# Kernel optimization log

Hardware: AMD Instinct MI355X
Metric: run time of the kernel (lower is better)

Reference implementation:

```python
import jax, jax.numpy as jnp
import numpy as np

V, D, H, L, DFF = 32000, 512, 8, 6, 2048
B, T = 64, 256
PAD_IDX = 1


def _pos_encoding(t, d):
    pos = jnp.arange(t, dtype=jnp.float32)[:, None]          # [t,1]
    i2 = jnp.arange(0, d, 2, dtype=jnp.float32)              # [d/2]
    ang = pos / jnp.power(10000.0, i2 / d)                   # [t,d/2]
    pe = jnp.zeros((t, d), dtype=jnp.float32)
    pe = pe.at[:, 0::2].set(jnp.sin(ang))
    pe = pe.at[:, 1::2].set(jnp.cos(ang))
    return pe


def _ln(x, g, b):
    mu = x.mean(-1, keepdims=True)
    var = ((x - mu) ** 2).mean(-1, keepdims=True)
    return (x - mu) * jax.lax.rsqrt(var + 1e-5) * g + b


def _mha(xq, xkv, Wq, Wk, Wv, Wo, bo, causal):
    b, tq, d = xq.shape
    tk = xkv.shape[1]
    hd = d // H
    q = (xq @ Wq).reshape(b, tq, H, hd)
    k = (xkv @ Wk).reshape(b, tk, H, hd)
    v = (xkv @ Wv).reshape(b, tk, H, hd)
    wei = jnp.einsum('bqhd,bkhd->bhqk', q, k) * (hd ** -0.5)
    if causal:
        mask = jnp.tril(jnp.ones((tq, tk), dtype=bool))
        wei = jnp.where(mask, wei, -jnp.inf)
    wei = jax.nn.softmax(wei, axis=-1)
    out = jnp.einsum('bhqk,bkhd->bqhd', wei, v).reshape(b, tq, d)
    return out @ Wo + bo


def _ffn(x, W1, b1, W2, b2):
    return jax.nn.relu(x @ W1 + b1) @ W2 + b2


def setup_inputs() -> dict:
    key = jax.random.key(0)
    ks = iter(jax.random.split(key, 64))
    nrm = lambda shape: (jax.random.normal(next(ks), shape, dtype=jnp.float32) * 0.02)
    inp = {
        'idx': jax.random.randint(next(ks), (B, T), 0, V),
        'idx_enc': jax.random.randint(next(ks), (B, T), 0, V),
        'targets': jax.random.randint(next(ks), (B, T), 0, V),
        'emb_dec': nrm((V, D)),
        'emb_enc': nrm((V, D)),
        # encoder stacks [L, ...]
        'enc_Wq': nrm((L, D, D)), 'enc_Wk': nrm((L, D, D)), 'enc_Wv': nrm((L, D, D)),
        'enc_Wo': nrm((L, D, D)), 'enc_bo': jnp.zeros((L, D)),
        'enc_ln_g': jnp.ones((L, 2, D)), 'enc_ln_b': jnp.zeros((L, 2, D)),
        'enc_W1': nrm((L, D, DFF)), 'enc_b1': jnp.zeros((L, DFF)),
        'enc_W2': nrm((L, DFF, D)), 'enc_b2': jnp.zeros((L, D)),
        # decoder stacks [L, ...]
        'dec_Wq_sa': nrm((L, D, D)), 'dec_Wk_sa': nrm((L, D, D)), 'dec_Wv_sa': nrm((L, D, D)),
        'dec_Wo_sa': nrm((L, D, D)), 'dec_bo_sa': jnp.zeros((L, D)),
        'dec_Wq_xa': nrm((L, D, D)), 'dec_Wk_xa': nrm((L, D, D)), 'dec_Wv_xa': nrm((L, D, D)),
        'dec_Wo_xa': nrm((L, D, D)), 'dec_bo_xa': jnp.zeros((L, D)),
        'dec_ln_g': jnp.ones((L, 4, D)), 'dec_ln_b': jnp.zeros((L, 4, D)),
        'dec_W1': nrm((L, D, DFF)), 'dec_b1': jnp.zeros((L, DFF)),
        'dec_W2': nrm((L, DFF, D)), 'dec_b2': jnp.zeros((L, D)),
        'lnf_g': jnp.ones((D,)), 'lnf_b': jnp.zeros((D,)),
        'Wlm': nrm((D, V)), 'blm': jnp.zeros((V,)),
    }
    return inp


def reference(idx, idx_enc, targets, emb_dec, emb_enc,
              enc_Wq, enc_Wk, enc_Wv, enc_Wo, enc_bo, enc_ln_g, enc_ln_b,
              enc_W1, enc_b1, enc_W2, enc_b2,
              dec_Wq_sa, dec_Wk_sa, dec_Wv_sa, dec_Wo_sa, dec_bo_sa,
              dec_Wq_xa, dec_Wk_xa, dec_Wv_xa, dec_Wo_xa, dec_bo_xa,
              dec_ln_g, dec_ln_b, dec_W1, dec_b1, dec_W2, dec_b2,
              lnf_g, lnf_b, Wlm, blm):
    t_dec = idx.shape[1]
    t_enc = idx_enc.shape[1]
    pe = _pos_encoding(256, D)
    # encoder
    y = emb_enc[idx_enc] + pe[:t_enc]
    for l in range(L):
        h = _ln(y, enc_ln_g[l, 0], enc_ln_b[l, 0])
        y = y + _mha(h, h, enc_Wq[l], enc_Wk[l], enc_Wv[l], enc_Wo[l], enc_bo[l], causal=False)
        h = _ln(y, enc_ln_g[l, 1], enc_ln_b[l, 1])
        y = y + _ffn(h, enc_W1[l], enc_b1[l], enc_W2[l], enc_b2[l])
    # decoder
    x = emb_dec[idx] + pe[:t_dec]
    for l in range(L):
        h = _ln(x, dec_ln_g[l, 0], dec_ln_b[l, 0])
        x = x + _mha(h, h, dec_Wq_sa[l], dec_Wk_sa[l], dec_Wv_sa[l], dec_Wo_sa[l], dec_bo_sa[l], causal=True)
        hq = _ln(x, dec_ln_g[l, 1], dec_ln_b[l, 1])
        hk = _ln(y, dec_ln_g[l, 2], dec_ln_b[l, 2])
        x = x + _mha(hq, hk, dec_Wq_xa[l], dec_Wk_xa[l], dec_Wv_xa[l], dec_Wo_xa[l], dec_bo_xa[l], causal=False)
        h = _ln(x, dec_ln_g[l, 3], dec_ln_b[l, 3])
        x = x + _ffn(h, dec_W1[l], dec_b1[l], dec_W2[l], dec_b2[l])
    x = _ln(x, lnf_g, lnf_b)
    logits = (x @ Wlm + blm).reshape(-1, V)  # [B*T, V]
    # cross entropy with ignore_index = PAD_IDX, mean over non-ignored
    tgt = targets.reshape(-1)
    logp = jax.nn.log_softmax(logits, axis=-1)
    nll = -jnp.take_along_axis(logp, tgt[:, None], axis=-1)[:, 0]
    valid = (tgt != PAD_IDX).astype(logits.dtype)
    loss = jnp.sum(nll * valid) / jnp.maximum(jnp.sum(valid), 1.0)
    return logits, loss
```

## Files before the change

kernel.cpp:

```cpp
#include <hip/hip_runtime.h>

typedef __attribute__((ext_vector_type(8))) short s8v;
typedef __attribute__((ext_vector_type(4))) float f4v;
using u16 = unsigned short;

__device__ __forceinline__ u16 f2bf(float f) {
  union { float f; unsigned u; } v; v.f = f;
  return (u16)((v.u + 0x7FFFu + ((v.u >> 16) & 1u)) >> 16);
}

__global__ __launch_bounds__(256) void pe_kernel(float* __restrict__ pe) {
  int i = blockIdx.x * 256 + threadIdx.x;
  int t = i >> 8, p = i & 255;
  float ex = (2.f * (float)p) / 512.f;
  float ang = (float)t * expf(-ex * 9.210340371976184f);
  pe[t * 512 + 2 * p]     = sinf(ang);
  pe[t * 512 + 2 * p + 1] = cosf(ang);
}

__global__ __launch_bounds__(256) void wconv_kernel(const float* __restrict__ in,
    u16* __restrict__ out, int R, int C, size_t dstride) {
  __shared__ float tile[64][65];
  const size_t mat = (size_t)R * C;
  const float* src = in + (size_t)blockIdx.z * mat;
  u16* dst = out + (size_t)blockIdx.z * dstride;
  int r0 = blockIdx.x * 64, c0 = blockIdx.y * 64;
  int tr = threadIdx.x >> 6, tc = threadIdx.x & 63;
#pragma unroll
  for (int i = 0; i < 16; ++i)
    tile[i * 4 + tr][tc] = src[(size_t)(r0 + i * 4 + tr) * C + (c0 + tc)];
  __syncthreads();
#pragma unroll
  for (int i = 0; i < 16; ++i)
    dst[(size_t)(c0 + i * 4 + tr) * R + (r0 + tc)] = f2bf(tile[tc][i * 4 + tr]);
}

struct WcSq { const float* src[12]; u16* dst[12]; unsigned long long dstr[12]; };
__global__ __launch_bounds__(256) void wconv_sq_kernel(WcSq S) {
  __shared__ float tile[64][65];
  int mm = blockIdx.z / 6, l = blockIdx.z % 6;
  const float* src = S.src[mm] + (size_t)l * 512 * 512;
  u16* dst = S.dst[mm] + (size_t)l * S.dstr[mm];
  int r0 = blockIdx.x * 64, c0 = blockIdx.y * 64;
  int tr = threadIdx.x >> 6, tc = threadIdx.x & 63;
#pragma unroll
  for (int i = 0; i < 16; ++i)
    tile[i * 4 + tr][tc] = src[(size_t)(r0 + i * 4 + tr) * 512 + (c0 + tc)];
  __syncthreads();
#pragma unroll
  for (int i = 0; i < 16; ++i)
    dst[(size_t)(c0 + i * 4 + tr) * 512 + (r0 + tc)] = f2bf(tile[tc][i * 4 + tr]);
}

__device__ __forceinline__ void ln_row(f4v v0, f4v v1, const float* g, const float* b,
                                       int lane, u16* outrow) {
  float s = v0[0] + v0[1] + v0[2] + v0[3] + v1[0] + v1[1] + v1[2] + v1[3];
#pragma unroll
  for (int o = 1; o < 64; o <<= 1) s += __shfl_xor(s, o);
  float mu = s * (1.f / 512.f);
  float q = 0.f;
#pragma unroll
  for (int j = 0; j < 4; ++j) {
    float d0 = v0[j] - mu; q += d0 * d0;
    float d1 = v1[j] - mu; q += d1 * d1;
  }
#pragma unroll
  for (int o = 1; o < 64; o <<= 1) q += __shfl_xor(q, o);
  float rs = rsqrtf(q * (1.f / 512.f) + 1e-5f);
  f4v g0 = *(const f4v*)(g + lane * 8), g1 = *(const f4v*)(g + lane * 8 + 4);
  f4v b0 = *(const f4v*)(b + lane * 8), b1 = *(const f4v*)(b + lane * 8 + 4);
  s8v ov;
#pragma unroll
  for (int j = 0; j < 4; ++j) {
    ov[j]     = (short)f2bf((v0[j] - mu) * rs * g0[j] + b0[j]);
    ov[4 + j] = (short)f2bf((v1[j] - mu) * rs * g1[j] + b1[j]);
  }
  *(s8v*)(outrow + lane * 8) = ov;
}

__global__ __launch_bounds__(256) void ln_kernel(const float* __restrict__ x,
    const float* __restrict__ g, const float* __restrict__ b, u16* __restrict__ out) {
  int row = blockIdx.x * 4 + (threadIdx.x >> 6);
  int lane = threadIdx.x & 63;
  const float* xr = x + (size_t)row * 512 + lane * 8;
  ln_row(*(const f4v*)xr, *(const f4v*)(xr + 4), g, b, lane, out + (size_t)row * 512);
}

__global__ __launch_bounds__(256) void ln2_kernel(
    const float* __restrict__ x1, const float* __restrict__ g1, const float* __restrict__ b1,
    u16* __restrict__ o1, const float* __restrict__ x2, const float* __restrict__ g2,
    const float* __restrict__ b2, u16* __restrict__ o2) {
  int row = blockIdx.x * 4 + (threadIdx.x >> 6);
  int lane = threadIdx.x & 63;
  const float* x = x1; const float* g = g1; const float* b = b1; u16* o = o1;
  if (row >= 16384) { row -= 16384; x = x2; g = g2; b = b2; o = o2; }
  const float* xr = x + (size_t)row * 512 + lane * 8;
  ln_row(*(const f4v*)xr, *(const f4v*)(xr + 4), g, b, lane, o + (size_t)row * 512);
}

__global__ __launch_bounds__(256) void emb_ln_kernel(const int* __restrict__ idx,
    const float* __restrict__ emb, const float* __restrict__ pe,
    const float* __restrict__ g, const float* __restrict__ b,
    float* __restrict__ y, u16* __restrict__ h) {
  int row = blockIdx.x * 4 + (threadIdx.x >> 6);
  int lane = threadIdx.x & 63;
  int tok = idx[row], t = row & 255;
  const float* e = emb + (size_t)tok * 512 + lane * 8;
  const float* p = pe + (size_t)t * 512 + lane * 8;
  f4v v0 = *(const f4v*)e + *(const f4v*)p;
  f4v v1 = *(const f4v*)(e + 4) + *(const f4v*)(p + 4);
  float* yr = y + (size_t)row * 512 + lane * 8;
  *(f4v*)yr = v0; *(f4v*)(yr + 4) = v1;
  ln_row(v0, v1, g, b, lane, h + (size_t)row * 512);
}

template<int HAS_BIAS, int ADD_RES, int RELU, int OUT_BF16, int WLOSS, int NT,
         int SWZM, int DUAL>
__global__ __launch_bounds__(256, 4) void gemm128(
    const u16* __restrict__ A, const u16* __restrict__ Bt,
    const float* __restrict__ bias, const float* __restrict__ res,
    void* __restrict__ outp, int M, int N, int K,
    float* __restrict__ pmax, float* __restrict__ psum,
    const u16* __restrict__ A2, const u16* __restrict__ Bt2,
    void* __restrict__ out2) {
  __shared__ __align__(16) u16 smem[2 * 128 * 64];
  u16* As = smem;
  u16* Bs = smem + 128 * 64;
  const int tid = threadIdx.x, lane = tid & 63, w = tid >> 6;
  int bx, by;
  if (SWZM == 1) {
    int flat = blockIdx.y * gridDim.x + blockIdx.x;
    int xcd = flat & 7, local = flat >> 3;
    int p = local / gridDim.y;
    by = local - p * gridDim.y;
    bx = xcd * (gridDim.x >> 3) + p;
  } else {
    int nx = gridDim.x;
    int flat = blockIdx.y * nx + blockIdx.x;
    int per = (nx * gridDim.y) >> 3;
    int sw = (flat & 7) * per + (flat >> 3);
    by = sw / nx; bx = sw - by * nx;
  }
  if (DUAL && by >= 4) { A = A2; Bt = Bt2; outp = out2; N = 1024; by -= 4; }
  const int m0 = bx * 128, n0 = by * 128;
  const int wm = (w >> 1) * 64, wn = (w & 1) * 64;
  const int lhi = lane >> 4, llo = lane & 15;
  const int srow = tid >> 3;
  const int sl = tid & 7;
  const int gcol = (sl ^ (srow & 7)) * 8;

  const u16* Ag = A + (size_t)(m0 + srow) * K + gcol;
  const u16* Bg = Bt + (size_t)(n0 + srow) * K + gcol;
  const size_t rstep = (size_t)32 * K;
  const int sx = llo & 7;

  f4v acc[4][4] = {};
  const int nk = K >> 6;
  for (int t = 0; t < nk; ++t) {
    const int kt = t * 64;
#pragma unroll
    for (int q = 0; q < 4; ++q)
      __builtin_amdgcn_global_load_lds(
          (const __attribute__((address_space(1))) void*)(Ag + q * rstep + kt),
          (__attribute__((address_space(3))) void*)(&As[(q * 32 + srow) * 64 + sl * 8]),
          16, 0, 0);
#pragma unroll
    for (int q = 0; q < 4; ++q)
      __builtin_amdgcn_global_load_lds(
          (const __attribute__((address_space(1))) void*)(Bg + q * rstep + kt),
          (__attribute__((address_space(3))) void*)(&Bs[(q * 32 + srow) * 64 + sl * 8]),
          16, 0, 0);
    __syncthreads();
#pragma unroll
    for (int kk = 0; kk < 2; ++kk) {
      s8v af[4], bfv[4];
#pragma unroll
      for (int i = 0; i < 4; ++i)
        af[i] = *(const s8v*)&As[(wm + i * 16 + llo) * 64 + (((kk * 4 + lhi) ^ sx) * 8)];
#pragma unroll
      for (int j = 0; j < 4; ++j)
        bfv[j] = *(const s8v*)&Bs[(wn + j * 16 + llo) * 64 + (((kk * 4 + lhi) ^ sx) * 8)];
#pragma unroll
      for (int i = 0; i < 4; ++i)
#pragma unroll
        for (int j = 0; j < 4; ++j)
          acc[i][j] = __builtin_amdgcn_mfma_f32_16x16x32_bf16(af[i], bfv[j], acc[i][j], 0, 0, 0);
    }
    __syncthreads();
  }

  if (OUT_BF16) {
    float bvj[4];
#pragma unroll
    for (int j = 0; j < 4; ++j)
      bvj[j] = HAS_BIAS ? bias[n0 + wn + j * 16 + llo] : 0.f;
#pragma unroll
    for (int i = 0; i < 4; ++i) {
#pragma unroll
      for (int j = 0; j < 4; ++j) {
        int col = n0 + wn + j * 16 + llo;
#pragma unroll
        for (int r = 0; r < 4; ++r) {
          int row = m0 + wm + i * 16 + lhi * 4 + r;
          float v = acc[i][j][r] + bvj[j];
          if (RELU) v = fmaxf(v, 0.f);
          ((u16*)outp)[(size_t)row * N + col] = f2bf(v);
        }
      }
    }
  } else {
    float* lb = (float*)smem;
    float* wbuf = lb + w * 1088;
    float* lbm = lb + 4608;
    float* lbs = lb + 4864;
    f4v bias4 = {0.f, 0.f, 0.f, 0.f};
    if (HAS_BIAS) bias4 = *(const f4v*)(bias + n0 + wn + llo * 4);
#pragma unroll
    for (int i = 0; i < 4; ++i) {
#pragma unroll
      for (int j = 0; j < 4; ++j)
#pragma unroll
        for (int r = 0; r < 4; ++r)
          wbuf[(lhi * 4 + r) * 68 + j * 16 + llo] = acc[i][j][r];
      asm volatile("s_waitcnt lgkmcnt(0)" ::: "memory");
      __builtin_amdgcn_sched_barrier(0);
#pragma unroll
      for (int p = 0; p < 4; ++p) {
        int r16 = p * 4 + lhi;
        f4v v4 = *(const f4v*)&wbuf[r16 * 68 + llo * 4];
        v4 += bias4;
        int grow = m0 + wm + i * 16 + r16;
        int gcol4 = n0 + wn + llo * 4;
        if (ADD_RES) v4 += *(const f4v*)(res + (size_t)grow * N + gcol4);
        if (RELU) {
          v4[0] = fmaxf(v4[0], 0.f); v4[1] = fmaxf(v4[1], 0.f);
          v4[2] = fmaxf(v4[2], 0.f); v4[3] = fmaxf(v4[3], 0.f);
        }
        float* dst = (float*)outp + (size_t)grow * N + gcol4;
        if (NT) __builtin_nontemporal_store(v4, (f4v*)dst);
        else    *(f4v*)dst = v4;
        if (WLOSS) {
          float mx = fmaxf(fmaxf(v4[0], v4[1]), fmaxf(v4[2], v4[3]));
          mx = fmaxf(mx, __shfl_xor(mx, 1));
          mx = fmaxf(mx, __shfl_xor(mx, 2));
          mx = fmaxf(mx, __shfl_xor(mx, 4));
          mx = fmaxf(mx, __shfl_xor(mx, 8));
          float sum = __expf(v4[0] - mx) + __expf(v4[1] - mx)
                    + __expf(v4[2] - mx) + __expf(v4[3] - mx);
          sum += __shfl_xor(sum, 1); sum += __shfl_xor(sum, 2);
          sum += __shfl_xor(sum, 4); sum += __shfl_xor(sum, 8);
          if (llo == 0) {
            int lr = wm + i * 16 + r16;
            lbm[lr * 2 + (wn >> 6)] = mx;
            lbs[lr * 2 + (wn >> 6)] = sum;
          }
        }
      }
      asm volatile("s_waitcnt lgkmcnt(0)" ::: "memory");
      __builtin_amdgcn_sched_barrier(0);
    }
    if (WLOSS) {
      __syncthreads();
      if (tid < 128) {
        float ma = lbm[tid * 2], mb = lbm[tid * 2 + 1];
        float sa = lbs[tid * 2], sb = lbs[tid * 2 + 1];
        float m = fmaxf(ma, mb);
        float ss = sa * __expf(ma - m) + sb * __expf(mb - m);
        int ntile = N >> 7;
        pmax[(size_t)(m0 + tid) * ntile + by] = m;
        psum[(size_t)(m0 + tid) * ntile + by] = ss;
      }
    }
  }
}

__global__ __launch_bounds__(256, 2) void attn_kernel(
    const u16* __restrict__ Qp, int qs, const u16* __restrict__ Kp,
    const u16* __restrict__ Vp, int kvs, u16* __restrict__ Ob, int causal) {
  __shared__ __align__(16) u16 Ks[64][72];
  __shared__ __align__(16) u16 Vt[64][66];
  __shared__ __align__(16) u16 Ps[4][16][66];
  const int tid = threadIdx.x, lane = tid & 63, w = tid >> 6;
  const int b = blockIdx.x >> 3, h = blockIdx.x & 7;
  const size_t qbase  = (size_t)b * 256 * qs  + (size_t)h * 64;
  const size_t kvbase = (size_t)b * 256 * kvs + (size_t)h * 64;
  const size_t obase  = (size_t)b * 256 * 512 + (size_t)h * 64;
  const int lhi = lane >> 4, llo = lane & 15;
  s8v aq0[4], aq1[4];
#pragma unroll
  for (int qc = 0; qc < 4; ++qc) {
    const u16* qp = Qp + qbase + (size_t)(w * 64 + qc * 16 + llo) * qs;
    aq0[qc] = *(const s8v*)(qp + lhi * 8);
    aq1[qc] = *(const s8v*)(qp + 32 + lhi * 8);
  }
  f4v o[4][4] = {};
  float mrow[16], lrow[16];
#pragma unroll
  for (int i = 0; i < 16; ++i) { mrow[i] = -1e30f; lrow[i] = 0.f; }

  for (int kt = 0; kt < 4; ++kt) {
    if (kt) __syncthreads();
    {
      int tr = tid >> 3, d0 = (tid & 7) * 8;
#pragma unroll
      for (int it = 0; it < 2; ++it) {
        int t = it * 32 + tr;
        const u16* kp = Kp + kvbase + (size_t)(kt * 64 + t) * kvs + d0;
        *(s8v*)&Ks[t][d0] = *(const s8v*)kp;
        s8v vv = *(const s8v*)(Vp + kvbase + (size_t)(kt * 64 + t) * kvs + d0);
#pragma unroll
        for (int j = 0; j < 8; ++j) Vt[d0 + j][t] = (u16)vv[j];
      }
    }
    __syncthreads();
#pragma unroll
    for (int qc = 0; qc < 4; ++qc) {
      if (causal && kt * 64 > w * 64 + qc * 16 + 15) continue;
      f4v S[4];
#pragma unroll
      for (int c = 0; c < 4; ++c) {
        s8v bk0 = *(const s8v*)&Ks[c * 16 + llo][lhi * 8];
        s8v bk1 = *(const s8v*)&Ks[c * 16 + llo][32 + lhi * 8];
        f4v z = {0.f, 0.f, 0.f, 0.f};
        z = __builtin_amdgcn_mfma_f32_16x16x32_bf16(aq0[qc], bk0, z, 0, 0, 0);
        S[c] = __builtin_amdgcn_mfma_f32_16x16x32_bf16(aq1[qc], bk1, z, 0, 0, 0);
      }
      float scv[4];
#pragma unroll
      for (int r = 0; r < 4; ++r) {
        const int tq = w * 64 + qc * 16 + lhi * 4 + r;
        float tmax = -1e30f;
#pragma unroll
        for (int c = 0; c < 4; ++c) {
          float s = S[c][r] * 0.125f;
          if (causal && (kt * 64 + c * 16 + llo) > tq) s = -1e30f;
          S[c][r] = s;
          tmax = fmaxf(tmax, s);
        }
        tmax = fmaxf(tmax, __shfl_xor(tmax, 1));
        tmax = fmaxf(tmax, __shfl_xor(tmax, 2));
        tmax = fmaxf(tmax, __shfl_xor(tmax, 4));
        tmax = fmaxf(tmax, __shfl_xor(tmax, 8));
        float mo = mrow[qc * 4 + r];
        float mn = fmaxf(mo, tmax);
        float sc = __expf(mo - mn);
        float sum = 0.f;
#pragma unroll
        for (int c = 0; c < 4; ++c) {
          float p = __expf(S[c][r] - mn);
          sum += p;
          Ps[w][lhi * 4 + r][c * 16 + llo] = f2bf(p);
        }
        sum += __shfl_xor(sum, 1); sum += __shfl_xor(sum, 2);
        sum += __shfl_xor(sum, 4); sum += __shfl_xor(sum, 8);
        lrow[qc * 4 + r] = lrow[qc * 4 + r] * sc + sum;
        mrow[qc * 4 + r] = mn;
        scv[r] = sc;
      }
#pragma unroll
      for (int nb = 0; nb < 4; ++nb)
#pragma unroll
        for (int r = 0; r < 4; ++r)
          o[qc][nb][r] *= scv[r];
      asm volatile("s_waitcnt lgkmcnt(0)" ::: "memory");
      __builtin_amdgcn_sched_barrier(0);
#pragma unroll
      for (int kb = 0; kb < 2; ++kb) {
        s8v pa = *(const s8v*)&Ps[w][llo][kb * 32 + lhi * 8];
#pragma unroll
        for (int nb = 0; nb < 4; ++nb) {
          s8v bv = *(const s8v*)&Vt[nb * 16 + llo][kb * 32 + lhi * 8];
          o[qc][nb] = __builtin_amdgcn_mfma_f32_16x16x32_bf16(pa, bv, o[qc][nb], 0, 0, 0);
        }
      }
    }
  }
#pragma unroll
  for (int qc = 0; qc < 4; ++qc)
#pragma unroll
    for (int nb = 0; nb < 4; ++nb)
#pragma unroll
      for (int r = 0; r < 4; ++r) {
        float inv = 1.f / lrow[qc * 4 + r];
        Ob[obase + (size_t)(w * 64 + qc * 16 + lhi * 4 + r) * 512 + nb * 16 + llo] =
            f2bf(o[qc][nb][r] * inv);
      }
}

__global__ __launch_bounds__(256) void loss_lse_kernel(const float* __restrict__ pmax,
    const float* __restrict__ psum, const float* __restrict__ logits,
    const int* __restrict__ tgt, float* __restrict__ nll, float* __restrict__ valid) {
  const int w = threadIdx.x >> 6, lane = threadIdx.x & 63;
  const int row = blockIdx.x * 4 + w;
  float m = -1e30f, s = 0.f;
  for (int e = lane; e < 250; e += 64) {
    float pm = pmax[(size_t)row * 250 + e], ps = psum[(size_t)row * 250 + e];
    if (pm > m) { s = s * __expf(m - pm) + ps; m = pm; }
    else          s += ps * __expf(pm - m);
  }
#pragma unroll
  for (int o = 1; o < 64; o <<= 1) {
    float om = __shfl_xor(m, o), os = __shfl_xor(s, o);
    float mm = fmaxf(m, om);
    s = s * __expf(m - mm) + os * __expf(om - mm);
    m = mm;
  }
  if (lane == 0) {
    int t = tgt[row];
    float lse = m + logf(s);
    float v = (t != 1) ? 1.f : 0.f;
    nll[row] = v * (lse - logits[(size_t)row * 32000 + t]);
    valid[row] = v;
  }
}

__global__ __launch_bounds__(256) void loss_final_kernel(const float* __restrict__ nll,
    const float* __restrict__ valid, float* __restrict__ out) {
  __shared__ float sa[256], sb[256];
  int tid = threadIdx.x;
  float s = 0.f, c = 0.f;
  for (int i = tid; i < 16384; i += 256) { s += nll[i]; c += valid[i]; }
  sa[tid] = s; sb[tid] = c;
  __syncthreads();
  for (int st = 128; st > 0; st >>= 1) {
    if (tid < st) { sa[tid] += sa[tid + st]; sb[tid] += sb[tid + st]; }
    __syncthreads();
  }
  if (tid == 0) out[0] = sa[0] / fmaxf(sb[0], 1.f);
}

extern "C" void kernel_launch(void* const* d_in, const int* in_sizes, int n_in,
                              void* d_out, int out_size, void* d_ws, size_t ws_size,
                              hipStream_t stream) {
  (void)in_sizes; (void)n_in; (void)out_size; (void)ws_size;
  const int* idx       = (const int*)d_in[0];
  const int* idx_enc   = (const int*)d_in[1];
  const int* targets   = (const int*)d_in[2];
  const float* emb_dec = (const float*)d_in[3];
  const float* emb_enc = (const float*)d_in[4];
  const float* enc_Wq  = (const float*)d_in[5];
  const float* enc_Wk  = (const float*)d_in[6];
  const float* enc_Wv  = (const float*)d_in[7];
  const float* enc_Wo  = (const float*)d_in[8];
  const float* enc_bo  = (const float*)d_in[9];
  const float* enc_ln_g = (const float*)d_in[10];
  const float* enc_ln_b = (const float*)d_in[11];
  const float* enc_W1  = (const float*)d_in[12];
  const float* enc_b1  = (const float*)d_in[13];
  const float* enc_W2  = (const float*)d_in[14];
  const float* enc_b2  = (const float*)d_in[15];
  const float* dWq_sa  = (const float*)d_in[16];
  const float* dWk_sa  = (const float*)d_in[17];
  const float* dWv_sa  = (const float*)d_in[18];
  const float* dWo_sa  = (const float*)d_in[19];
  const float* dbo_sa  = (const float*)d_in[20];
  const float* dWq_xa  = (const float*)d_in[21];
  const float* dWk_xa  = (const float*)d_in[22];
  const float* dWv_xa  = (const float*)d_in[23];
  const float* dWo_xa  = (const float*)d_in[24];
  const float* dbo_xa  = (const float*)d_in[25];
  const float* dec_ln_g = (const float*)d_in[26];
  const float* dec_ln_b = (const float*)d_in[27];
  const float* dec_W1  = (const float*)d_in[28];
  const float* dec_b1  = (const float*)d_in[29];
  const float* dec_W2  = (const float*)d_in[30];
  const float* dec_b2  = (const float*)d_in[31];
  const float* lnf_g   = (const float*)d_in[32];
  const float* lnf_b   = (const float*)d_in[33];
  const float* Wlm     = (const float*)d_in[34];
  const float* blm     = (const float*)d_in[35];
  float* out_logits = (float*)d_out;
  float* out_loss   = out_logits + (size_t)16384 * 32000;

  size_t off = 0;
  auto alloc = [&](size_t bytes) -> char* {
    char* p = (char*)d_ws + off;
    off += (bytes + 255) & ~(size_t)255;
    return p;
  };
  const size_t SQ = 512 * 512, SF = 512 * 2048;
  u16* tWqkvE = (u16*)alloc(6 * 3 * SQ * 2);
  u16* tWoE   = (u16*)alloc(6 * SQ * 2);
  u16* tW1E   = (u16*)alloc(6 * SF * 2);
  u16* tW2E   = (u16*)alloc(6 * SF * 2);
  u16* tWqkvS = (u16*)alloc(6 * 3 * SQ * 2);
  u16* tWoS   = (u16*)alloc(6 * SQ * 2);
  u16* tWqX   = (u16*)alloc(6 * SQ * 2);
  u16* tWkvX  = (u16*)alloc(6 * 2 * SQ * 2);
  u16* tWoX   = (u16*)alloc(6 * SQ * 2);
  u16* tW1D   = (u16*)alloc(6 * SF * 2);
  u16* tW2D   = (u16*)alloc(6 * SF * 2);
  u16* tWlm   = (u16*)alloc((size_t)32000 * 512 * 2);
  float* pe   = (float*)alloc(256 * 512 * 4);
  float* yE   = (float*)alloc((size_t)16384 * 512 * 4);
  float* xD   = (float*)alloc((size_t)16384 * 512 * 4);
  u16* hA     = (u16*)alloc((size_t)16384 * 512 * 2);
  u16* hB     = (u16*)alloc((size_t)16384 * 512 * 2);
  u16* qkvB   = (u16*)alloc((size_t)16384 * 1536 * 2);
  u16* qB     = (u16*)alloc((size_t)16384 * 512 * 2);
  u16* kvB    = (u16*)alloc((size_t)16384 * 1024 * 2);
  u16* atB    = (u16*)alloc((size_t)16384 * 512 * 2);
  u16* midB   = (u16*)alloc((size_t)16384 * 2048 * 2);
  float* pmax = (float*)alloc((size_t)16384 * 250 * 4);
  float* psum = (float*)alloc((size_t)16384 * 250 * 4);
  float* rnll = (float*)alloc(16384 * 4);
  float* rval = (float*)alloc(16384 * 4);

  dim3 tb(256);
  const size_t S3 = 3 * SQ, S2 = 2 * SQ;
  {
    WcSq S;
    S.src[0] = enc_Wq;  S.dst[0] = tWqkvE + 0 * SQ; S.dstr[0] = S3;
    S.src[1] = enc_Wk;  S.dst[1] = tWqkvE + 1 * SQ; S.dstr[1] = S3;
    S.src[2] = enc_Wv;  S.dst[2] = tWqkvE + 2 * SQ; S.dstr[2] = S3;
    S.src[3] = enc_Wo;  S.dst[3] = tWoE;            S.dstr[3] = SQ;
    S.src[4] = dWq_sa;  S.dst[4] = tWqkvS + 0 * SQ; S.dstr[4] = S3;
    S.src[5] = dWk_sa;  S.dst[5] = tWqkvS + 1 * SQ; S.dstr[5] = S3;
    S.src[6] = dWv_sa;  S.dst[6] = tWqkvS + 2 * SQ; S.dstr[6] = S3;
    S.src[7] = dWo_sa;  S.dst[7] = tWoS;            S.dstr[7] = SQ;
    S.src[8] = dWq_xa;  S.dst[8] = tWqX;            S.dstr[8] = SQ;
    S.src[9] = dWk_xa;  S.dst[9] = tWkvX + 0 * SQ;  S.dstr[9] = S2;
    S.src[10] = dWv_xa; S.dst[10] = tWkvX + 1 * SQ; S.dstr[10] = S2;
    S.src[11] = dWo_xa; S.dst[11] = tWoX;           S.dstr[11] = SQ;
    wconv_sq_kernel<<<dim3(8, 8, 72), tb, 0, stream>>>(S);
  }
  wconv_kernel<<<dim3(8, 32, 6), tb, 0, stream>>>(enc_W1, tW1E, 512, 2048, SF);
  wconv_kernel<<<dim3(32, 8, 6), tb, 0, stream>>>(enc_W2, tW2E, 2048, 512, SF);
  wconv_kernel<<<dim3(8, 32, 6), tb, 0, stream>>>(dec_W1, tW1D, 512, 2048, SF);
  wconv_kernel<<<dim3(32, 8, 6), tb, 0, stream>>>(dec_W2, tW2D, 2048, 512, SF);
  wconv_kernel<<<dim3(8, 500, 1), tb, 0, stream>>>(Wlm, tWlm, 512, 32000, (size_t)0);
  pe_kernel<<<256, 256, 0, stream>>>(pe);

  auto ln = [&](const float* xin, const float* g, const float* bb, u16* o) {
    ln_kernel<<<4096, 256, 0, stream>>>(xin, g, bb, o);
  };
  auto g_bf16 = [&](const u16* Ap, const u16* Bp, u16* Op, int N) {
    gemm128<0, 0, 0, 1, 0, 0, 0, 0><<<dim3(128, N / 128), 256, 0, stream>>>(
        Ap, Bp, nullptr, nullptr, Op, 16384, N, 512, nullptr, nullptr,
        nullptr, nullptr, nullptr);
  };
  auto g_qkv_x = [&](const u16* Aq, const u16* Bq, u16* Oq,
                     const u16* Akv, const u16* Bkv, u16* Okv) {
    gemm128<0, 0, 0, 1, 0, 0, 0, 1><<<dim3(128, 12), 256, 0, stream>>>(
        Aq, Bq, nullptr, nullptr, Oq, 16384, 512, 512, nullptr, nullptr,
        Akv, Bkv, Okv);
  };
  auto proj_res = [&](const u16* Ap, const u16* Bp, const float* bi, float* xr, int K) {
    gemm128<1, 1, 0, 0, 0, 0, 0, 0><<<dim3(128, 4), 256, 0, stream>>>(
        Ap, Bp, bi, xr, xr, 16384, 512, K, nullptr, nullptr,
        nullptr, nullptr, nullptr);
  };
  auto ffn1 = [&](const u16* Ap, const u16* Bp, const float* bi, u16* Op) {
    gemm128<1, 0, 1, 1, 0, 0, 0, 0><<<dim3(128, 16), 256, 0, stream>>>(
        Ap, Bp, bi, nullptr, Op, 16384, 2048, 512, nullptr, nullptr,
        nullptr, nullptr, nullptr);
  };

  emb_ln_kernel<<<4096, 256, 0, stream>>>(idx_enc, emb_enc, pe,
      enc_ln_g + 0, enc_ln_b + 0, yE, hA);
  for (int l = 0; l < 6; ++l) {
    if (l) ln(yE, enc_ln_g + (l * 2 + 0) * 512, enc_ln_b + (l * 2 + 0) * 512, hA);
    g_bf16(hA, tWqkvE + l * S3, qkvB, 1536);
    attn_kernel<<<512, 256, 0, stream>>>(qkvB, 1536, qkvB + 512, qkvB + 1024, 1536, atB, 0);
    proj_res(atB, tWoE + l * SQ, enc_bo + l * 512, yE, 512);
    ln(yE, enc_ln_g + (l * 2 + 1) * 512, enc_ln_b + (l * 2 + 1) * 512, hA);
    ffn1(hA, tW1E + l * SF, enc_b1 + l * 2048, midB);
    proj_res(midB, tW2E + l * SF, enc_b2 + l * 512, yE, 2048);
  }

  emb_ln_kernel<<<4096, 256, 0, stream>>>(idx, emb_dec, pe,
      dec_ln_g + 0, dec_ln_b + 0, xD, hA);
  for (int l = 0; l < 6; ++l) {
    if (l) ln(xD, dec_ln_g + (l * 4 + 0) * 512, dec_ln_b + (l * 4 + 0) * 512, hA);
    g_bf16(hA, tWqkvS + l * S3, qkvB, 1536);
    attn_kernel<<<512, 256, 0, stream>>>(qkvB, 1536, qkvB + 512, qkvB + 1024, 1536, atB, 1);
    proj_res(atB, tWoS + l * SQ, dbo_sa + l * 512, xD, 512);
    ln2_kernel<<<8192, 256, 0, stream>>>(
        xD, dec_ln_g + (l * 4 + 1) * 512, dec_ln_b + (l * 4 + 1) * 512, hA,
        yE, dec_ln_g + (l * 4 + 2) * 512, dec_ln_b + (l * 4 + 2) * 512, hB);
    g_qkv_x(hA, tWqX + l * SQ, qB, hB, tWkvX + l * S2, kvB);
    attn_kernel<<<512, 256, 0, stream>>>(qB, 512, kvB, kvB + 512, 1024, atB, 0);
    proj_res(atB, tWoX + l * SQ, dbo_xa + l * 512, xD, 512);
    ln(xD, dec_ln_g + (l * 4 + 3) * 512, dec_ln_b + (l * 4 + 3) * 512, hA);
    ffn1(hA, tW1D + l * SF, dec_b1 + l * 2048, midB);
    proj_res(midB, tW2D + l * SF, dec_b2 + l * 512, xD, 2048);
  }

  ln(xD, lnf_g, lnf_b, hA);
  gemm128<1, 0, 0, 0, 1, 1, 1, 0><<<dim3(128, 250), 256, 0, stream>>>(
      hA, tWlm, blm, nullptr, out_logits, 16384, 32000, 512, pmax, psum,
      nullptr, nullptr, nullptr);
  loss_lse_kernel<<<4096, 256, 0, stream>>>(pmax, psum, out_logits, targets, rnll, rval);
  loss_final_kernel<<<1, 256, 0, stream>>>(rnll, rval, out_loss);
}
```

Baseline: 4.836 ms.

## Run output projections and FFN GEMMs in FP8 with FP8 activations

Converts the Wo, W1 and W2 weights to FP8 (e4m3) and makes the attention output, the pre-FFN layernorm output and the FFN hidden activations FP8. The matching GEMMs now use a new FP8 MFMA path with a smaller shared-memory tile. This is meant to halve memory traffic for those operands and use the higher FP8 matrix throughput. In exchange it loses precision: there is no scaling, so small values go subnormal or flush, which may break the accuracy tolerance on logits and loss.

```diff
diff --git a/kernel.cpp b/kernel.cpp
--- a/kernel.cpp
+++ b/kernel.cpp
@@ -3,10 +3,28 @@
 typedef __attribute__((ext_vector_type(8))) short s8v;
 typedef __attribute__((ext_vector_type(4))) float f4v;
 using u16 = unsigned short;
+using u8 = unsigned char;
 
 __device__ __forceinline__ u16 f2bf(float f) {
   union { float f; unsigned u; } v; v.f = f;
   return (u16)((v.u + 0x7FFFu + ((v.u >> 16) & 1u)) >> 16);
+}
+
+__device__ __forceinline__ u8 f2f8(float f) {
+  union { float f; unsigned u; } v; v.f = f;
+  unsigned s = (v.u >> 24) & 0x80;
+  v.u &= 0x7fffffff;
+  if (!(v.f < 448.f)) return (u8)(s | 0x7e);
+  if (v.f < 0.015625f) {
+    int q = (int)(v.f * 512.f + 0.5f);
+    return (u8)(s | (unsigned)q);
+  }
+  unsigned u = v.u + 0x7FFFFu + ((v.u >> 20) & 1u);
+  int e = (int)(u >> 23) - 127;
+  unsigned m = (u >> 20) & 7u;
+  unsigned code = ((unsigned)(e + 7) << 3) | m;
+  if (code > 0x7e) code = 0x7e;
+  return (u8)(s | code);
 }
 
 __global__ __launch_bounds__(256) void pe_kernel(float* __restrict__ pe) {
@@ -18,12 +36,12 @@
   pe[t * 512 + 2 * p + 1] = cosf(ang);
 }
 
+template<int FP8>
 __global__ __launch_bounds__(256) void wconv_kernel(const float* __restrict__ in,
-    u16* __restrict__ out, int R, int C, size_t dstride) {
+    void* __restrict__ out, int R, int C, size_t dstride) {
   __shared__ float tile[64][65];
   const size_t mat = (size_t)R * C;
   const float* src = in + (size_t)blockIdx.z * mat;
-  u16* dst = out + (size_t)blockIdx.z * dstride;
   int r0 = blockIdx.x * 64, c0 = blockIdx.y * 64;
   int tr = threadIdx.x >> 6, tc = threadIdx.x & 63;
 #pragma unroll
@@ -31,16 +49,20 @@
     tile[i * 4 + tr][tc] = src[(size_t)(r0 + i * 4 + tr) * C + (c0 + tc)];
   __syncthreads();
 #pragma unroll
-  for (int i = 0; i < 16; ++i)
-    dst[(size_t)(c0 + i * 4 + tr) * R + (r0 + tc)] = f2bf(tile[tc][i * 4 + tr]);
-}
-
-struct WcSq { const float* src[12]; u16* dst[12]; unsigned long long dstr[12]; };
+  for (int i = 0; i < 16; ++i) {
+    size_t di = (size_t)(c0 + i * 4 + tr) * R + (r0 + tc);
+    float val = tile[tc][i * 4 + tr];
+    if (FP8) ((u8*)out + (size_t)blockIdx.z * dstride)[di] = f2f8(val);
+    else     ((u16*)out + (size_t)blockIdx.z * dstride)[di] = f2bf(val);
+  }
+}
+
+struct WcSq { const float* src[12]; void* dst[12]; unsigned long long dstr[12]; unsigned fp8m; };
 __global__ __launch_bounds__(256) void wconv_sq_kernel(WcSq S) {
   __shared__ float tile[64][65];
   int mm = blockIdx.z / 6, l = blockIdx.z % 6;
   const float* src = S.src[mm] + (size_t)l * 512 * 512;
-  u16* dst = S.dst[mm] + (size_t)l * S.dstr[mm];
+  int fp8 = (S.fp8m >> mm) & 1;
   int r0 = blockIdx.x * 64, c0 = blockIdx.y * 64;
   int tr = threadIdx.x >> 6, tc = threadIdx.x & 63;
 #pragma unroll
@@ -48,12 +70,17 @@
     tile[i * 4 + tr][tc] = src[(size_t)(r0 + i * 4 + tr) * 512 + (c0 + tc)];
   __syncthreads();
 #pragma unroll
-  for (int i = 0; i < 16; ++i)
-    dst[(size_t)(c0 + i * 4 + tr) * 512 + (r0 + tc)] = f2bf(tile[tc][i * 4 + tr]);
-}
-
+  for (int i = 0; i < 16; ++i) {
+    size_t di = (size_t)(c0 + i * 4 + tr) * 512 + (r0 + tc);
+    float val = tile[tc][i * 4 + tr];
+    if (fp8) ((u8*)S.dst[mm] + (size_t)l * S.dstr[mm])[di] = f2f8(val);
+    else     ((u16*)S.dst[mm] + (size_t)l * S.dstr[mm])[di] = f2bf(val);
+  }
+}
+
+template<int FP8>
 __device__ __forceinline__ void ln_row(f4v v0, f4v v1, const float* g, const float* b,
-                                       int lane, u16* outrow) {
+                                       int lane, void* outrow) {
   float s = v0[0] + v0[1] + v0[2] + v0[3] + v1[0] + v1[1] + v1[2] + v1[3];
 #pragma unroll
   for (int o = 1; o < 64; o <<= 1) s += __shfl_xor(s, o);
@@ -69,21 +96,34 @@
   float rs = rsqrtf(q * (1.f / 512.f) + 1e-5f);
   f4v g0 = *(const f4v*)(g + lane * 8), g1 = *(const f4v*)(g + lane * 8 + 4);
   f4v b0 = *(const f4v*)(b + lane * 8), b1 = *(const f4v*)(b + lane * 8 + 4);
-  s8v ov;
-#pragma unroll
-  for (int j = 0; j < 4; ++j) {
-    ov[j]     = (short)f2bf((v0[j] - mu) * rs * g0[j] + b0[j]);
-    ov[4 + j] = (short)f2bf((v1[j] - mu) * rs * g1[j] + b1[j]);
-  }
-  *(s8v*)(outrow + lane * 8) = ov;
-}
-
+  if (FP8) {
+    unsigned long long ov = 0;
+#pragma unroll
+    for (int j = 0; j < 4; ++j) {
+      ov |= (unsigned long long)f2f8((v0[j] - mu) * rs * g0[j] + b0[j]) << (8 * j);
+      ov |= (unsigned long long)f2f8((v1[j] - mu) * rs * g1[j] + b1[j]) << (8 * (4 + j));
+    }
+    *(unsigned long long*)((u8*)outrow + lane * 8) = ov;
+  } else {
+    s8v ov;
+#pragma unroll
+    for (int j = 0; j < 4; ++j) {
+      ov[j]     = (short)f2bf((v0[j] - mu) * rs * g0[j] + b0[j]);
+      ov[4 + j] = (short)f2bf((v1[j] - mu) * rs * g1[j] + b1[j]);
+    }
+    *(s8v*)((u16*)outrow + lane * 8) = ov;
+  }
+}
+
+template<int FP8>
 __global__ __launch_bounds__(256) void ln_kernel(const float* __restrict__ x,
-    const float* __restrict__ g, const float* __restrict__ b, u16* __restrict__ out) {
+    const float* __restrict__ g, const float* __restrict__ b, void* __restrict__ out) {
   int row = blockIdx.x * 4 + (threadIdx.x >> 6);
   int lane = threadIdx.x & 63;
   const float* xr = x + (size_t)row * 512 + lane * 8;
-  ln_row(*(const f4v*)xr, *(const f4v*)(xr + 4), g, b, lane, out + (size_t)row * 512);
+  void* orow = FP8 ? (void*)((u8*)out + (size_t)row * 512)
+                   : (void*)((u16*)out + (size_t)row * 512);
+  ln_row<FP8>(*(const f4v*)xr, *(const f4v*)(xr + 4), g, b, lane, orow);
 }
 
 __global__ __launch_bounds__(256) void ln2_kernel(
@@ -95,7 +135,7 @@
   const float* x = x1; const float* g = g1; const float* b = b1; u16* o = o1;
   if (row >= 16384) { row -= 16384; x = x2; g = g2; b = b2; o = o2; }
   const float* xr = x + (size_t)row * 512 + lane * 8;
-  ln_row(*(const f4v*)xr, *(const f4v*)(xr + 4), g, b, lane, o + (size_t)row * 512);
+  ln_row<0>(*(const f4v*)xr, *(const f4v*)(xr + 4), g, b, lane, o + (size_t)row * 512);
 }
 
 __global__ __launch_bounds__(256) void emb_ln_kernel(const int* __restrict__ idx,
@@ -111,21 +151,20 @@
   f4v v1 = *(const f4v*)(e + 4) + *(const f4v*)(p + 4);
   float* yr = y + (size_t)row * 512 + lane * 8;
   *(f4v*)yr = v0; *(f4v*)(yr + 4) = v1;
-  ln_row(v0, v1, g, b, lane, h + (size_t)row * 512);
-}
-
-template<int HAS_BIAS, int ADD_RES, int RELU, int OUT_BF16, int WLOSS, int NT,
-         int SWZM, int DUAL>
+  ln_row<0>(v0, v1, g, b, lane, h + (size_t)row * 512);
+}
+
+template<int AB8, int OMODE, int HAS_BIAS, int ADD_RES, int RELU, int WLOSS,
+         int NT, int SWZM, int DUAL>
 __global__ __launch_bounds__(256, 4) void gemm128(
-    const u16* __restrict__ A, const u16* __restrict__ Bt,
+    const void* __restrict__ Av, const void* __restrict__ Btv,
     const float* __restrict__ bias, const float* __restrict__ res,
     void* __restrict__ outp, int M, int N, int K,
     float* __restrict__ pmax, float* __restrict__ psum,
-    const u16* __restrict__ A2, const u16* __restrict__ Bt2,
+    const void* __restrict__ A2, const void* __restrict__ Bt2,
     void* __restrict__ out2) {
-  __shared__ __align__(16) u16 smem[2 * 128 * 64];
-  u16* As = smem;
-  u16* Bs = smem + 128 * 64;
+  constexpr int SMEM_BYTES = AB8 ? 20480 : 32768;
+  __shared__ __align__(16) u8 smem[SMEM_BYTES];
   const int tid = threadIdx.x, lane = tid & 63, w = tid >> 6;
   int bx, by;
   if (SWZM == 1) {
@@ -141,55 +180,100 @@
     int sw = (flat & 7) * per + (flat >> 3);
     by = sw / nx; bx = sw - by * nx;
   }
-  if (DUAL && by >= 4) { A = A2; Bt = Bt2; outp = out2; N = 1024; by -= 4; }
+  const void* Ause = Av; const void* Buse = Btv; void* Ouse = outp;
+  int Nn = N;
+  if (DUAL && by >= 4) { Ause = A2; Buse = Bt2; Ouse = out2; Nn = 1024; by -= 4; }
   const int m0 = bx * 128, n0 = by * 128;
   const int wm = (w >> 1) * 64, wn = (w & 1) * 64;
   const int lhi = lane >> 4, llo = lane & 15;
-  const int srow = tid >> 3;
-  const int sl = tid & 7;
-  const int gcol = (sl ^ (srow & 7)) * 8;
-
-  const u16* Ag = A + (size_t)(m0 + srow) * K + gcol;
-  const u16* Bg = Bt + (size_t)(n0 + srow) * K + gcol;
-  const size_t rstep = (size_t)32 * K;
-  const int sx = llo & 7;
 
   f4v acc[4][4] = {};
   const int nk = K >> 6;
-  for (int t = 0; t < nk; ++t) {
-    const int kt = t * 64;
-#pragma unroll
-    for (int q = 0; q < 4; ++q)
-      __builtin_amdgcn_global_load_lds(
-          (const __attribute__((address_space(1))) void*)(Ag + q * rstep + kt),
-          (__attribute__((address_space(3))) void*)(&As[(q * 32 + srow) * 64 + sl * 8]),
-          16, 0, 0);
-#pragma unroll
-    for (int q = 0; q < 4; ++q)
-      __builtin_amdgcn_global_load_lds(
-          (const __attribute__((address_space(1))) void*)(Bg + q * rstep + kt),
-          (__attribute__((address_space(3))) void*)(&Bs[(q * 32 + srow) * 64 + sl * 8]),
-          16, 0, 0);
-    __syncthreads();
-#pragma unroll
-    for (int kk = 0; kk < 2; ++kk) {
-      s8v af[4], bfv[4];
-#pragma unroll
-      for (int i = 0; i < 4; ++i)
-        af[i] = *(const s8v*)&As[(wm + i * 16 + llo) * 64 + (((kk * 4 + lhi) ^ sx) * 8)];
-#pragma unroll
-      for (int j = 0; j < 4; ++j)
-        bfv[j] = *(const s8v*)&Bs[(wn + j * 16 + llo) * 64 + (((kk * 4 + lhi) ^ sx) * 8)];
-#pragma unroll
-      for (int i = 0; i < 4; ++i)
+
+  if (AB8) {
+    const u8* A = (const u8*)Ause;
+    const u8* Bt = (const u8*)Buse;
+    u8* As8 = smem;
+    u8* Bs8 = smem + 8192;
+    const int r = tid >> 2, s16 = tid & 3;
+    const int sxb = (llo & 3) << 1;
+    for (int t = 0; t < nk; ++t) {
+      const int kt = t * 64;
+#pragma unroll
+      for (int q = 0; q < 2; ++q) {
+        int row = q * 64 + r;
+        int gofs = kt + ((s16 ^ (row & 3)) * 16);
+        __builtin_amdgcn_global_load_lds(
+            (const __attribute__((address_space(1))) void*)(A + (size_t)(m0 + row) * K + gofs),
+            (__attribute__((address_space(3))) void*)(&As8[row * 64 + s16 * 16]), 16, 0, 0);
+        __builtin_amdgcn_global_load_lds(
+            (const __attribute__((address_space(1))) void*)(Bt + (size_t)(n0 + row) * K + gofs),
+            (__attribute__((address_space(3))) void*)(&Bs8[row * 64 + s16 * 16]), 16, 0, 0);
+      }
+      __syncthreads();
+#pragma unroll
+      for (int kk = 0; kk < 2; ++kk) {
+        long af[4], bf8[4];
+#pragma unroll
+        for (int i = 0; i < 4; ++i)
+          af[i] = *(const long*)&As8[(wm + i * 16 + llo) * 64 + (((kk * 4 + lhi) ^ sxb) * 8)];
 #pragma unroll
         for (int j = 0; j < 4; ++j)
-          acc[i][j] = __builtin_amdgcn_mfma_f32_16x16x32_bf16(af[i], bfv[j], acc[i][j], 0, 0, 0);
-    }
-    __syncthreads();
-  }
-
-  if (OUT_BF16) {
+          bf8[j] = *(const long*)&Bs8[(wn + j * 16 + llo) * 64 + (((kk * 4 + lhi) ^ sxb) * 8)];
+#pragma unroll
+        for (int i = 0; i < 4; ++i)
+#pragma unroll
+          for (int j = 0; j < 4; ++j)
+            acc[i][j] = __builtin_amdgcn_mfma_f32_16x16x32_fp8_fp8(af[i], bf8[j], acc[i][j], 0, 0, 0);
+      }
+      __syncthreads();
+    }
+  } else {
+    const u16* A = (const u16*)Ause;
+    const u16* Bt = (const u16*)Buse;
+    u16* As = (u16*)smem;
+    u16* Bs = (u16*)(smem + 16384);
+    const int srow = tid >> 3, sl = tid & 7;
+    const int gcol = (sl ^ (srow & 7)) * 8;
+    const u16* Ag = A + (size_t)(m0 + srow) * K + gcol;
+    const u16* Bg = Bt + (size_t)(n0 + srow) * K + gcol;
+    const size_t rstep = (size_t)32 * K;
+    const int sx = llo & 7;
+    for (int t = 0; t < nk; ++t) {
+      const int kt = t * 64;
+#pragma unroll
+      for (int q = 0; q < 4; ++q)
+        __builtin_amdgcn_global_load_lds(
+            (const __attribute__((address_space(1))) void*)(Ag + q * rstep + kt),
+            (__attribute__((address_space(3))) void*)(&As[(q * 32 + srow) * 64 + sl * 8]),
+            16, 0, 0);
+#pragma unroll
+      for (int q = 0; q < 4; ++q)
+        __builtin_amdgcn_global_load_lds(
+            (const __attribute__((address_space(1))) void*)(Bg + q * rstep + kt),
+            (__attribute__((address_space(3))) void*)(&Bs[(q * 32 + srow) * 64 + sl * 8]),
+            16, 0, 0);
+      __syncthreads();
+#pragma unroll
+      for (int kk = 0; kk < 2; ++kk) {
+        s8v af[4], bfv[4];
+#pragma unroll
+        for (int i = 0; i < 4; ++i)
+          af[i] = *(const s8v*)&As[(wm + i * 16 + llo) * 64 + (((kk * 4 + lhi) ^ sx) * 8)];
+#pragma unroll
+        for (int j = 0; j < 4; ++j)
+          bfv[j] = *(const s8v*)&Bs[(wn + j * 16 + llo) * 64 + (((kk * 4 + lhi) ^ sx) * 8)];
+#pragma unroll
+        for (int i = 0; i < 4; ++i)
+#pragma unroll
+          for (int j = 0; j < 4; ++j)
+            acc[i][j] = __builtin_amdgcn_mfma_f32_16x16x32_bf16(af[i], bfv[j], acc[i][j], 0, 0, 0);
+      }
+      __syncthreads();
+    }
+  }
+
+  if (OMODE == 1 || OMODE == 2) {
     float bvj[4];
 #pragma unroll
     for (int j = 0; j < 4; ++j)
@@ -204,7 +288,8 @@
           int row = m0 + wm + i * 16 + lhi * 4 + r;
           float v = acc[i][j][r] + bvj[j];
           if (RELU) v = fmaxf(v, 0.f);
-          ((u16*)outp)[(size_t)row * N + col] = f2bf(v);
+          if (OMODE == 1) ((u16*)Ouse)[(size_t)row * Nn + col] = f2bf(v);
+          else            ((u8*)Ouse)[(size_t)row * Nn + col] = f2f8(v);
         }
       }
     }
@@ -231,12 +316,12 @@
         v4 += bias4;
         int grow = m0 + wm + i * 16 + r16;
         int gcol4 = n0 + wn + llo * 4;
-        if (ADD_RES) v4 += *(const f4v*)(res + (size_t)grow * N + gcol4);
+        if (ADD_RES) v4 += *(const f4v*)(res + (size_t)grow * Nn + gcol4);
         if (RELU) {
           v4[0] = fmaxf(v4[0], 0.f); v4[1] = fmaxf(v4[1], 0.f);
           v4[2] = fmaxf(v4[2], 0.f); v4[3] = fmaxf(v4[3], 0.f);
         }
-        float* dst = (float*)outp + (size_t)grow * N + gcol4;
+        float* dst = (float*)Ouse + (size_t)grow * Nn + gcol4;
         if (NT) __builtin_nontemporal_store(v4, (f4v*)dst);
         else    *(f4v*)dst = v4;
         if (WLOSS) {
@@ -266,7 +351,7 @@
         float sa = lbs[tid * 2], sb = lbs[tid * 2 + 1];
         float m = fmaxf(ma, mb);
         float ss = sa * __expf(ma - m) + sb * __expf(mb - m);
-        int ntile = N >> 7;
+        int ntile = Nn >> 7;
         pmax[(size_t)(m0 + tid) * ntile + by] = m;
         psum[(size_t)(m0 + tid) * ntile + by] = ss;
       }
@@ -276,7 +361,7 @@
 
 __global__ __launch_bounds__(256, 2) void attn_kernel(
     const u16* __restrict__ Qp, int qs, const u16* __restrict__ Kp,
-    const u16* __restrict__ Vp, int kvs, u16* __restrict__ Ob, int causal) {
+    const u16* __restrict__ Vp, int kvs, u8* __restrict__ Ob, int causal) {
   __shared__ __align__(16) u16 Ks[64][72];
   __shared__ __align__(16) u16 Vt[64][66];
   __shared__ __align__(16) u16 Ps[4][16][66];
@@ -383,7 +468,7 @@
       for (int r = 0; r < 4; ++r) {
         float inv = 1.f / lrow[qc * 4 + r];
         Ob[obase + (size_t)(w * 64 + qc * 16 + lhi * 4 + r) * 512 + nb * 16 + llo] =
-            f2bf(o[qc][nb][r] * inv);
+            f2f8(o[qc][nb][r] * inv);
       }
 }
 
@@ -480,16 +565,16 @@
   };
   const size_t SQ = 512 * 512, SF = 512 * 2048;
   u16* tWqkvE = (u16*)alloc(6 * 3 * SQ * 2);
-  u16* tWoE   = (u16*)alloc(6 * SQ * 2);
-  u16* tW1E   = (u16*)alloc(6 * SF * 2);
-  u16* tW2E   = (u16*)alloc(6 * SF * 2);
+  u8*  tWoE   = (u8*)alloc(6 * SQ);
+  u8*  tW1E   = (u8*)alloc(6 * SF);
+  u8*  tW2E   = (u8*)alloc(6 * SF);
   u16* tWqkvS = (u16*)alloc(6 * 3 * SQ * 2);
-  u16* tWoS   = (u16*)alloc(6 * SQ * 2);
+  u8*  tWoS   = (u8*)alloc(6 * SQ);
   u16* tWqX   = (u16*)alloc(6 * SQ * 2);
   u16* tWkvX  = (u16*)alloc(6 * 2 * SQ * 2);
-  u16* tWoX   = (u16*)alloc(6 * SQ * 2);
-  u16* tW1D   = (u16*)alloc(6 * SF * 2);
-  u16* tW2D   = (u16*)alloc(6 * SF * 2);
+  u8*  tWoX   = (u8*)alloc(6 * SQ);
+  u8*  tW1D   = (u8*)alloc(6 * SF);
+  u8*  tW2D   = (u8*)alloc(6 * SF);
   u16* tWlm   = (u16*)alloc((size_t)32000 * 512 * 2);
   float* pe   = (float*)alloc(256 * 512 * 4);
   float* yE   = (float*)alloc((size_t)16384 * 512 * 4);
@@ -499,8 +584,8 @@
   u16* qkvB   = (u16*)alloc((size_t)16384 * 1536 * 2);
   u16* qB     = (u16*)alloc((size_t)16384 * 512 * 2);
   u16* kvB    = (u16*)alloc((size_t)16384 * 1024 * 2);
-  u16* atB    = (u16*)alloc((size_t)16384 * 512 * 2);
-  u16* midB   = (u16*)alloc((size_t)16384 * 2048 * 2);
+  u8*  atB    = (u8*)alloc((size_t)16384 * 512);
+  u8*  midB   = (u8*)alloc((size_t)16384 * 2048);
   float* pmax = (float*)alloc((size_t)16384 * 250 * 4);
   float* psum = (float*)alloc((size_t)16384 * 250 * 4);
   float* rnll = (float*)alloc(16384 * 4);
@@ -522,36 +607,40 @@
     S.src[9] = dWk_xa;  S.dst[9] = tWkvX + 0 * SQ;  S.dstr[9] = S2;
     S.src[10] = dWv_xa; S.dst[10] = tWkvX + 1 * SQ; S.dstr[10] = S2;
     S.src[11] = dWo_xa; S.dst[11] = tWoX;           S.dstr[11] = SQ;
+    S.fp8m = (1u << 3) | (1u << 7) | (1u << 11);
     wconv_sq_kernel<<<dim3(8, 8, 72), tb, 0, stream>>>(S);
   }
-  wconv_kernel<<<dim3(8, 32, 6), tb, 0, stream>>>(enc_W1, tW1E, 512, 2048, SF);
-  wconv_kernel<<<dim3(32, 8, 6), tb, 0, stream>>>(enc_W2, tW2E, 2048, 512, SF);
-  wconv_kernel<<<dim3(8, 32, 6), tb, 0, stream>>>(dec_W1, tW1D, 512, 2048, SF);
-  wconv_kernel<<<dim3(32, 8, 6), tb, 0, stream>>>(dec_W2, tW2D, 2048, 512, SF);
-  wconv_kernel<<<dim3(8, 500, 1), tb, 0, stream>>>(Wlm, tWlm, 512, 32000, (size_t)0);
+  wconv_kernel<1><<<dim3(8, 32, 6), tb, 0, stream>>>(enc_W1, tW1E, 512, 2048, SF);
+  wconv_kernel<1><<<dim3(32, 8, 6), tb, 0, stream>>>(enc_W2, tW2E, 2048, 512, SF);
+  wconv_kernel<1><<<dim3(8, 32, 6), tb, 0, stream>>>(dec_W1, tW1D, 512, 2048, SF);
+  wconv_kernel<1><<<dim3(32, 8, 6), tb, 0, stream>>>(dec_W2, tW2D, 2048, 512, SF);
+  wconv_kernel<0><<<dim3(8, 500, 1), tb, 0, stream>>>(Wlm, tWlm, 512, 32000, (size_t)0);
   pe_kernel<<<256, 256, 0, stream>>>(pe);
 
-  auto ln = [&](const float* xin, const float* g, const float* bb, u16* o) {
-    ln_kernel<<<4096, 256, 0, stream>>>(xin, g, bb, o);
+  auto ln16 = [&](const float* xin, const float* g, const float* bb, u16* o) {
+    ln_kernel<0><<<4096, 256, 0, stream>>>(xin, g, bb, o);
+  };
+  auto ln8 = [&](const float* xin, const float* g, const float* bb, void* o) {
+    ln_kernel<1><<<4096, 256, 0, stream>>>(xin, g, bb, o);
   };
   auto g_bf16 = [&](const u16* Ap, const u16* Bp, u16* Op, int N) {
-    gemm128<0, 0, 0, 1, 0, 0, 0, 0><<<dim3(128, N / 128), 256, 0, stream>>>(
+    gemm128<0, 1, 0, 0, 0, 0, 0, 0, 0><<<dim3(128, N / 128), 256, 0, stream>>>(
         Ap, Bp, nullptr, nullptr, Op, 16384, N, 512, nullptr, nullptr,
         nullptr, nullptr, nullptr);
   };
   auto g_qkv_x = [&](const u16* Aq, const u16* Bq, u16* Oq,
                      const u16* Akv, const u16* Bkv, u16* Okv) {
-    gemm128<0, 0, 0, 1, 0, 0, 0, 1><<<dim3(128, 12), 256, 0, stream>>>(
+    gemm128<0, 1, 0, 0, 0, 0, 0, 0, 1><<<dim3(128, 12), 256, 0, stream>>>(
         Aq, Bq, nullptr, nullptr, Oq, 16384, 512, 512, nullptr, nullptr,
         Akv, Bkv, Okv);
   };
-  auto proj_res = [&](const u16* Ap, const u16* Bp, const float* bi, float* xr, int K) {
-    gemm128<1, 1, 0, 0, 0, 0, 0, 0><<<dim3(128, 4), 256, 0, stream>>>(
+  auto proj_res8 = [&](const u8* Ap, const u8* Bp, const float* bi, float* xr, int K) {
+    gemm128<1, 0, 1, 1, 0, 0, 0, 0, 0><<<dim3(128, 4), 256, 0, stream>>>(
         Ap, Bp, bi, xr, xr, 16384, 512, K, nullptr, nullptr,
         nullptr, nullptr, nullptr);
   };
-  auto ffn1 = [&](const u16* Ap, const u16* Bp, const float* bi, u16* Op) {
-    gemm128<1, 0, 1, 1, 0, 0, 0, 0><<<dim3(128, 16), 256, 0, stream>>>(
+  auto ffn1_8 = [&](const u8* Ap, const u8* Bp, const float* bi, u8* Op) {
+    gemm128<1, 2, 1, 0, 1, 0, 0, 0, 0><<<dim3(128, 16), 256, 0, stream>>>(
         Ap, Bp, bi, nullptr, Op, 16384, 2048, 512, nullptr, nullptr,
         nullptr, nullptr, nullptr);
   };
@@ -559,35 +648,35 @@
   emb_ln_kernel<<<4096, 256, 0, stream>>>(idx_enc, emb_enc, pe,
       enc_ln_g + 0, enc_ln_b + 0, yE, hA);
   for (int l = 0; l < 6; ++l) {
-    if (l) ln(yE, enc_ln_g + (l * 2 + 0) * 512, enc_ln_b + (l * 2 + 0) * 512, hA);
+    if (l) ln16(yE, enc_ln_g + (l * 2 + 0) * 512, enc_ln_b + (l * 2 + 0) * 512, hA);
     g_bf16(hA, tWqkvE + l * S3, qkvB, 1536);
     attn_kernel<<<512, 256, 0, stream>>>(qkvB, 1536, qkvB + 512, qkvB + 1024, 1536, atB, 0);
-    proj_res(atB, tWoE + l * SQ, enc_bo + l * 512, yE, 512);
-    ln(yE, enc_ln_g + (l * 2 + 1) * 512, enc_ln_b + (l * 2 + 1) * 512, hA);
-    ffn1(hA, tW1E + l * SF, enc_b1 + l * 2048, midB);
-    proj_res(midB, tW2E + l * SF, enc_b2 + l * 512, yE, 2048);
+    proj_res8(atB, tWoE + l * SQ, enc_bo + l * 512, yE, 512);
+    ln8(yE, enc_ln_g + (l * 2 + 1) * 512, enc_ln_b + (l * 2 + 1) * 512, hA);
+    ffn1_8((const u8*)hA, tW1E + l * SF, enc_b1 + l * 2048, midB);
+    proj_res8(midB, tW2E + l * SF, enc_b2 + l * 512, yE, 2048);
   }
 
   emb_ln_kernel<<<4096, 256, 0, stream>>>(idx, emb_dec, pe,
       dec_ln_g + 0, dec_ln_b + 0, xD, hA);
   for (int l = 0; l < 6; ++l) {
-    if (l) ln(xD, dec_ln_g + (l * 4 + 0) * 512, dec_ln_b + (l * 4 + 0) * 512, hA);
+    if (l) ln16(xD, dec_ln_g + (l * 4 + 0) * 512, dec_ln_b + (l * 4 + 0) * 512, hA);
     g_bf16(hA, tWqkvS + l * S3, qkvB, 1536);
     attn_kernel<<<512, 256, 0, stream>>>(qkvB, 1536, qkvB + 512, qkvB + 1024, 1536, atB, 1);
-    proj_res(atB, tWoS + l * SQ, dbo_sa + l * 512, xD, 512);
+    proj_res8(atB, tWoS + l * SQ, dbo_sa + l * 512, xD, 512);
     ln2_kernel<<<8192, 256, 0, stream>>>(
         xD, dec_ln_g + (l * 4 + 1) * 512, dec_ln_b + (l * 4 + 1) * 512, hA,
         yE, dec_ln_g + (l * 4 + 2) * 512, dec_ln_b + (l * 4 + 2) * 512, hB);
     g_qkv_x(hA, tWqX + l * SQ, qB, hB, tWkvX + l * S2, kvB);
     attn_kernel<<<512, 256, 0, stream>>>(qB, 512, kvB, kvB + 512, 1024, atB, 0);
-    proj_res(atB, tWoX + l * SQ, dbo_xa + l * 512, xD, 512);
-    ln(xD, dec_ln_g + (l * 4 + 3) * 512, dec_ln_b + (l * 4 + 3) * 512, hA);
-    ffn1(hA, tW1D + l * SF, dec_b1 + l * 2048, midB);
-    proj_res(midB, tW2D + l * SF, dec_b2 + l * 512, xD, 2048);
-  }
-
-  ln(xD, lnf_g, lnf_b, hA);
-  gemm128<1, 0, 0, 0, 1, 1, 1, 0><<<dim3(128, 250), 256, 0, stream>>>(
+    proj_res8(atB, tWoX + l * SQ, dbo_xa + l * 512, xD, 512);
+    ln8(xD, dec_ln_g + (l * 4 + 3) * 512, dec_ln_b + (l * 4 + 3) * 512, hA);
+    ffn1_8((const u8*)hA, tW1D + l * SF, dec_b1 + l * 2048, midB);
+    proj_res8(midB, tW2D + l * SF, dec_b2 + l * 512, xD, 2048);
+  }
+
+  ln16(xD, lnf_g, lnf_b, hA);
+  gemm128<0, 0, 1, 0, 0, 1, 1, 1, 0><<<dim3(128, 250), 256, 0, stream>>>(
       hA, tWlm, blm, nullptr, out_logits, 16384, 32000, 512, pmax, psum,
       nullptr, nullptr, nullptr);
   loss_lse_kernel<<<4096, 256, 0, stream>>>(pmax, psum, out_logits, targets, rnll, rval);
```

After: 4.700 ms. -2.8%, faster.
